# Optimization experiments

Hardware: AMD Instinct MI355X
Metric: run time of the kernel (lower is better)

## Reference

```python
import jax, jax.numpy as jnp
import numpy as np

B, L, E, H, W = 2, 8192, 1024, 16, 128
HD = E // H  # 64


def setup_inputs() -> dict:
    key = jax.random.key(0)
    ks = jax.random.split(key, 9)
    s = 1.0 / np.sqrt(E)
    inp = {"x": jax.random.normal(ks[0], (B, L, E), jnp.float32)}
    for i, n in enumerate(["Wq", "Wk", "Wv", "Wo"]):
        inp[n] = jax.random.uniform(ks[1 + i], (E, E), jnp.float32, -s, s)
    for i, n in enumerate(["bq", "bk", "bv", "bo"]):
        inp[n] = jax.random.uniform(ks[5 + i], (E,), jnp.float32, -s, s)
    return inp


def _skew_prob(p, w):
    # (..., w, 2w+1) -> (..., w, 3w) with row i right-shifted by i:
    # out[..., i, i+j] = p[..., i, j]  (zeros elsewhere)
    lead = p.shape[:-2]
    M, Lc = p.shape[-2], p.shape[-1]
    p = jnp.pad(p, [(0, 0)] * len(lead) + [(0, 0), (0, M + 1)])
    p = p.reshape(*lead, M * (Lc + M + 1))[..., :-M].reshape(*lead, M, M + Lc)
    return p[..., :-1]


def _sliding_attend(q, k, v, w):
    # q,k,v: (b,h,l,d); banded attention, window w on each side (2w+1 diagonals)
    b, h, l, d = q.shape
    c = l // w
    qc = q.reshape(b, h, c, w, d)
    # per-chunk key/value windows of 3w tokens (w halo each side, zero padded)
    idx = jnp.arange(c)[:, None] * w + jnp.arange(3 * w)[None, :]  # (c, 3w)
    kw = jnp.pad(k, ((0, 0), (0, 0), (w, w), (0, 0)))[:, :, idx]  # (b,h,c,3w,d)
    s = jnp.einsum('bhcqd,bhckd->bhcqk', qc, kw)  # (b,h,c,w,3w)
    # extract band: band[i, j] = s[i, i+j], j in [0, 2w] (offset d = j - w)
    gidx = (jnp.arange(w)[:, None] + jnp.arange(2 * w + 1)[None, :])[None, None, None]
    band = jnp.take_along_axis(s, gidx, axis=-1).reshape(b, h, l, 2 * w + 1)
    # mask out-of-range positions (matches the module's edge -inf loop)
    pos = jnp.arange(l)[:, None] + (jnp.arange(2 * w + 1) - w)[None, :]
    band = jnp.where((pos >= 0) & (pos < l), band, -jnp.inf)
    prob = jax.nn.softmax(band / np.sqrt(d), axis=-1)  # scale by sqrt(head_dim)
    vw = jnp.pad(v, ((0, 0), (0, 0), (w, w), (0, 0)))[:, :, idx]  # (b,h,c,3w,d)
    p3 = _skew_prob(prob.reshape(b, h, c, w, 2 * w + 1), w)  # (b,h,c,w,3w)
    ctx = jnp.einsum('bhcqk,bhckd->bhcqd', p3, vw)
    return ctx.reshape(b, h, l, d)


def reference(x, Wq, Wk, Wv, Wo, bq, bk, bv, bo):
    q = (x @ Wq.T + bq).reshape(B, L, H, HD).transpose(0, 2, 1, 3)
    k = (x @ Wk.T + bk).reshape(B, L, H, HD).transpose(0, 2, 1, 3)
    v = (x @ Wv.T + bv).reshape(B, L, H, HD).transpose(0, 2, 1, 3)
    ctx = _sliding_attend(q, k, v, W)
    ctx = ctx.transpose(0, 2, 1, 3).reshape(B, L, E)
    return ctx @ Wo.T + bo
```

## Files before the change

kernel.cpp:

```cpp
#include <hip/hip_runtime.h>
#include <math.h>

#define B_SZ  2
#define L_SEQ 8192
#define EMB   1024
#define NH    16
#define HDIM  64
#define WIN   128
#define MROWS (B_SZ*L_SEQ)

typedef __attribute__((ext_vector_type(8))) _Float16 f16x8;
typedef __attribute__((ext_vector_type(4))) _Float16 f16x4;
typedef __attribute__((ext_vector_type(4))) float f32x4;

__device__ __forceinline__ void gload16(const void* g, void* l) {
    __builtin_amdgcn_global_load_lds(
        (const __attribute__((address_space(1))) unsigned int*)g,
        (__attribute__((address_space(3))) unsigned int*)l, 16, 0, 0);
}

__global__ __launch_bounds__(256)
void round_all(const float* __restrict__ x,
               const float* __restrict__ wq, const float* __restrict__ wk,
               const float* __restrict__ wv, const float* __restrict__ wo,
               _Float16* __restrict__ xf, _Float16* __restrict__ q16,
               _Float16* __restrict__ k16, _Float16* __restrict__ v16,
               _Float16* __restrict__ o16)
{
    const size_t NX = (size_t)MROWS * EMB, NW = (size_t)EMB * EMB;
    size_t gid = ((size_t)blockIdx.x * 256 + threadIdx.x) * 4;
    const float* src; _Float16* dst; size_t off;
    if (gid < NX)               { src = x;  dst = xf;  off = gid; }
    else if (gid < NX + NW)     { src = wq; dst = q16; off = gid - NX; }
    else if (gid < NX + 2*NW)   { src = wk; dst = k16; off = gid - NX - 2*NW + NW; }
    else if (gid < NX + 3*NW)   { src = wv; dst = v16; off = gid - NX - 2*NW; }
    else                        { src = wo; dst = o16; off = gid - NX - 3*NW; }
    float4 v = *(const float4*)(src + off);
    f16x4 o;
    o[0] = (_Float16)v.x; o[1] = (_Float16)v.y;
    o[2] = (_Float16)v.z; o[3] = (_Float16)v.w;
    *(f16x4*)(dst + off) = o;
}


#define STAGE_HT(ptr_, tb_, op_, h_, kt_)                                      \
    {                                                                          \
        char* d_ = smem + (op_) * 65536 + ((kt_) & 1) * 32768 + (h_) * 16384 + ldst; \
        const _Float16* s_ = (ptr_) + ((size_t)((tb_) + (h_) * 128 + srow6)) * 1024 + (kt_) * 64 + gch; \
        gload16(s_, d_);                                                       \
        gload16(s_ + 64 * 1024, d_ + 8192);                                    \
    }

#define DSREAD_A(qr_)                                                          \
    _Pragma("unroll")                                                          \
    for (int i_ = 0; i_ < 4; ++i_) {                                           \
        const int ro_ = (qr_) * 8192 + (i_ * 16 + frow) * 128;                 \
        af[i_][0] = *(const f16x8*)(Ab + ro_ + sb0);                           \
        af[i_][1] = *(const f16x8*)(Ab + ro_ + sb1);                           \
    }

#define DSREAD_B_TO(dst_, qc_)                                                 \
    _Pragma("unroll")                                                          \
    for (int j_ = 0; j_ < 2; ++j_) {                                           \
        const int ro_ = (brow + (qc_) * 32 + j_ * 16 + frow) * 128;            \
        dst_[j_][0] = *(const f16x8*)(Bb + ro_ + sb0);                         \
        dst_[j_][1] = *(const f16x8*)(Bb + ro_ + sb1);                         \
    }

#define MFMA16(qr_, qc_, barr_)                                                \
    __builtin_amdgcn_s_setprio(1);                                             \
    _Pragma("unroll")                                                          \
    for (int ks_ = 0; ks_ < 2; ++ks_)                                          \
        _Pragma("unroll")                                                      \
        for (int i_ = 0; i_ < 4; ++i_)                                         \
            _Pragma("unroll")                                                  \
            for (int j_ = 0; j_ < 2; ++j_)                                     \
                acc[(qr_) * 4 + i_][(qc_) * 2 + j_] =                          \
                    __builtin_amdgcn_mfma_f32_16x16x32_f16(                    \
                        af[i_][ks_], barr_[j_][ks_],                           \
                        acc[(qr_) * 4 + i_][(qc_) * 2 + j_], 0, 0, 0);         \
    __builtin_amdgcn_s_setprio(0);

#define BARM()                                                                 \
    asm volatile("" ::: "memory");                                             \
    __builtin_amdgcn_s_barrier();                                              \
    asm volatile("" ::: "memory");

#define GEMM8_CORE(Aptr, Bptr)                                                 \
    const int t = threadIdx.x;                                                 \
    const int wave = t >> 6, lane = t & 63;                                    \
    const int wr = wave >> 2, wc = wave & 3;                                   \
    const int frow = lane & 15, quad = lane >> 4;                              \
    const int srow6 = t >> 3;                                                  \
    const int gch = ((t & 7) ^ (srow6 & 7)) * 8;                               \
    const int ldst = t * 16;                                                   \
    const int sb0 = (quad ^ (frow & 7)) * 16, sb1 = sb0 ^ 64;                  \
    const int brow = (wc & 1) * 64;                                            \
    f32x4 acc[8][4] = {};                                                      \
    f16x8 af[4][2], bfA[2][2], bfB[2][2];                                      \
    STAGE_HT(Aptr, bm, 0, 0, 0) STAGE_HT(Aptr, bm, 0, 1, 0)                    \
    STAGE_HT(Bptr, bn, 1, 0, 0) STAGE_HT(Bptr, bn, 1, 1, 0)                    \
    for (int kt = 0; kt < 16; ++kt) {                                          \
        const char* Ab = smem + (kt & 1) * 32768 + wr * 16384;                 \
        const char* Bb = smem + 65536 + (kt & 1) * 32768 + (wc >> 1) * 16384;  \
        if (kt < 15) {                                                         \
            STAGE_HT(Aptr, bm, 0, 0, kt + 1)                                   \
            asm volatile("s_waitcnt vmcnt(2)" ::: "memory");                   \
        } else {                                                               \
            asm volatile("s_waitcnt vmcnt(0)" ::: "memory");                   \
        }                                                                      \
        BARM()                                                                 \
        DSREAD_A(0) DSREAD_B_TO(bfA, 0)          \
        MFMA16(0, 0, bfA)                                                      \
        DSREAD_B_TO(bfB, 1)                    \
        if (kt < 15) STAGE_HT(Aptr, bm, 0, 1, kt + 1)                          \
        BARM()                                                                 \
        MFMA16(0, 1, bfB)                                                      \
        DSREAD_A(1)                                                            \
        if (kt < 15) STAGE_HT(Bptr, bn, 1, 0, kt + 1)                          \
        BARM()                                                                 \
        MFMA16(1, 1, bfB)                                                      \
        if (kt < 15) STAGE_HT(Bptr, bn, 1, 1, kt + 1)                          \
        BARM()                                                                 \
        MFMA16(1, 0, bfA)                     \
        BARM()                                                                 \
    }

__global__ __launch_bounds__(512, 2)
void gemm_qkv(const _Float16* __restrict__ X,
              const _Float16* __restrict__ Wq, const _Float16* __restrict__ Wk,
              const _Float16* __restrict__ Wv,
              const float* __restrict__ bq, const float* __restrict__ bk,
              const float* __restrict__ bv,
              _Float16* __restrict__ qf, _Float16* __restrict__ kf,
              _Float16* __restrict__ vtf)
{
    __shared__ __attribute__((aligned(16))) char smem[131072];

    const int id = blockIdx.x;
    const int row = (id / 96) * 8 + (id & 7);
    const int colq = (id >> 3) % 12;
    const int wsel = colq >> 2;
    const int bm = row * 256, bn = (colq & 3) * 256;
    const _Float16* Bw = wsel == 0 ? Wq : wsel == 1 ? Wk : Wv;
    const float* bias = wsel == 0 ? bq : wsel == 1 ? bk : bv;
    const float scale = wsel == 0 ? 0.18033688011112042f : 1.0f;

    GEMM8_CORE(X, Bw)

    char* Cw = smem + wave * 8192;
    const int bb = bm >> 13;
    const int l0 = (bm & (L_SEQ - 1)) + wr * 128;
    const int h = (bn >> 6) + wc;
    if (wsel < 2) {
        _Float16* dst = wsel == 0 ? qf : kf;
        const size_t hb = ((size_t)(bb * NH + h)) * L_SEQ * HDIM;
        #pragma unroll
        for (int ih = 0; ih < 2; ++ih) {
            asm volatile("" ::: "memory");
            #pragma unroll
            for (int i = 0; i < 4; ++i)
                #pragma unroll
                for (int j = 0; j < 4; ++j) {
                    const int lc = j * 16 + frow;
                    const float bvv = bias[bn + wc * 64 + lc];
                    #pragma unroll
                    for (int r = 0; r < 4; ++r) {
                        const int lr = i * 16 + quad * 4 + r;
                        const int bo = lr * 128 + ((lc * 2) ^ ((lr & 7) << 4));
                        *(_Float16*)(Cw + bo) = (_Float16)((acc[ih * 4 + i][j][r] + bvv) * scale);
                    }
                }
            asm volatile("" ::: "memory");
            #pragma unroll
            for (int p = 0; p < 8; ++p) {
                const int idx = p * 64 + lane;
                const int lr = idx >> 3, seg = idx & 7;
                const int bo = lr * 128 + ((seg * 16) ^ ((lr & 7) << 4));
                uint4 v = *(const uint4*)(Cw + bo);
                *(uint4*)&dst[hb + (size_t)(l0 + ih * 64 + lr) * HDIM + seg * 8] = v;
            }
        }
    } else {
        const size_t hb = ((size_t)(bb * NH + h)) * HDIM * L_SEQ;
        #pragma unroll
        for (int ih = 0; ih < 2; ++ih) {
            asm volatile("" ::: "memory");
            #pragma unroll
            for (int i = 0; i < 4; ++i)
                #pragma unroll
                for (int j = 0; j < 4; ++j) {
                    const int lc = j * 16 + frow;
                    const float bvv = bias[bn + wc * 64 + lc];
                    #pragma unroll
                    for (int r = 0; r < 4; ++r) {
                        const int lr = i * 16 + quad * 4 + r;
                        const int bo = lc * 128 + ((lr * 2) ^ ((lc & 7) << 4));
                        *(_Float16*)(Cw + bo) = (_Float16)(acc[ih * 4 + i][j][r] + bvv);
                    }
                }
            asm volatile("" ::: "memory");
            #pragma unroll
            for (int p = 0; p < 8; ++p) {
                const int idx = p * 64 + lane;
                const int dc = idx >> 3, sl = idx & 7;
                const int bo = dc * 128 + ((sl * 16) ^ ((dc & 7) << 4));
                uint4 v = *(const uint4*)(Cw + bo);
                *(uint4*)&vtf[hb + (size_t)dc * L_SEQ + (l0 + ih * 64 + sl * 8)] = v;
            }
        }
    }
}

__global__ __launch_bounds__(512, 2)
void gemm_out(const _Float16* __restrict__ A, const _Float16* __restrict__ Bwm,
              const float* __restrict__ bias, float* __restrict__ C)
{
    constexpr int N = EMB;
    __shared__ __attribute__((aligned(16))) char smem[131072];

    const int id = blockIdx.x;
    const int row = (id / 32) * 8 + (id & 7);
    const int bm = row * 256, bn = ((id >> 3) & 3) * 256;

    GEMM8_CORE(A, Bwm)

    #pragma unroll
    for (int i = 0; i < 8; ++i) {
        int m0 = bm + wr * 128 + i * 16 + quad * 4;
        #pragma unroll
        for (int j = 0; j < 4; ++j) {
            int n = bn + wc * 64 + j * 16 + frow;
            float bvv = bias[n];
            #pragma unroll
            for (int r = 0; r < 4; ++r)
                C[(size_t)(m0 + r) * N + n] = acc[i][j][r] + bvv;
        }
    }
}

__global__ __launch_bounds__(1024)
void attn_mfma(const _Float16* __restrict__ qf, const _Float16* __restrict__ kf,
               const _Float16* __restrict__ vtf, _Float16* __restrict__ cf)
{
    __shared__ _Float16 Kt[8][4096];
    __shared__ _Float16 Vt[8][4096];

    const int t = threadIdx.x;
    const int wave = t >> 6, lane = t & 63;
    const int col = lane & 15, quad = lane >> 4;
    const int bh = blockIdx.y;
    const int xi = blockIdx.x;
    const int xq = (xi & 7) * 4 + (xi >> 3);
    const int q0 = xq * 256;
    const int oo = wave * 16;

    const int tk = t & 511;
    const int srow = tk >> 3, sc = tk & 7;
    const int gq = sc ^ (srow & 7);
    #pragma unroll
    for (int kt = 0; kt < 8; kt++) {
        const int p0s = q0 - WIN + kt * 64;
        if (p0s < 0 || p0s > L_SEQ - 64) continue;
        if (t < 512) {
            size_t kgi = ((size_t)bh * L_SEQ + p0s + srow) * HDIM + gq * 8;
            gload16(kf + kgi, (char*)&Kt[kt][0] + tk * 16);
        } else {
            size_t vgi = ((size_t)bh * HDIM + srow) * L_SEQ + p0s + gq * 8;
            gload16(vtf + vgi, (char*)&Vt[kt][0] + tk * 16);
        }
    }

    f16x8 qfr[2];
    {
        size_t qidx = ((size_t)bh * L_SEQ + q0 + oo + col) * HDIM + quad * 8;
        qfr[0] = *(const f16x8*)(qf + qidx);
        qfr[1] = *(const f16x8*)(qf + qidx + 32);
    }

    asm volatile("s_waitcnt vmcnt(0)" ::: "memory");
    __builtin_amdgcn_s_barrier();
    asm volatile("" ::: "memory");

    f32x4 o[4] = {};
    f32x4 o5 = {};
    const f16x4 vones = {(_Float16)1.0f, (_Float16)1.0f,
                         (_Float16)1.0f, (_Float16)1.0f};

    #pragma unroll
    for (int kt = 0; kt < 8; kt++) {
        const int p0 = q0 - WIN + kt * 64;
        if (p0 < 0 || p0 > L_SEQ - 64) continue;
        const int relp = kt * 64 - WIN - oo;
        if (relp < -191 || relp > 143) continue;

        const char* Kb = (const char*)&Kt[kt][0];
        const char* Vb = (const char*)&Vt[kt][0];

        f32x4 sT[4] = {};
        __builtin_amdgcn_s_setprio(1);
        #pragma unroll
        for (int ks = 0; ks < 2; ks++)
            #pragma unroll
            for (int n = 0; n < 4; n++) {
                int off = (n * 16 + col) * 128 + (((ks * 4 + quad) ^ (col & 7)) * 16);
                f16x8 kfr = *(const f16x8*)(Kb + off);
                sT[n] = __builtin_amdgcn_mfma_f32_16x16x32_f16(kfr, qfr[ks], sT[n], 0, 0, 0);
            }
        __builtin_amdgcn_s_setprio(0);
        if (relp < -113 || relp > 65) {
            const int qrow = q0 + oo + col;
            #pragma unroll
            for (int n = 0; n < 4; n++)
                #pragma unroll
                for (int r = 0; r < 4; r++) {
                    int dlt = (p0 + n * 16 + quad * 4 + r) - qrow;
                    if (dlt < -WIN || dlt > WIN) sT[n][r] = -3e38f;
                }
        }
        f16x4 pT[4];
        #pragma unroll
        for (int n = 0; n < 4; n++)
            #pragma unroll
            for (int r = 0; r < 4; r++)
                pT[n][r] = (_Float16)__builtin_amdgcn_exp2f(sT[n][r]);
        __builtin_amdgcn_s_setprio(1);
        #pragma unroll
        for (int n = 0; n < 4; n++)
            o5 = __builtin_amdgcn_mfma_f32_16x16x16f16(vones, pT[n], o5, 0, 0, 0);
        #pragma unroll
        for (int m = 0; m < 4; m++) {
            #pragma unroll
            for (int n = 0; n < 4; n++) {
                int off = (m * 16 + col) * 128 +
                          (((2 * n + (quad >> 1)) ^ (col & 7)) * 16) + (quad & 1) * 8;
                f16x4 vfr = *(const f16x4*)(Vb + off);
                o[m] = __builtin_amdgcn_mfma_f32_16x16x16f16(vfr, pT[n], o[m], 0, 0, 0);
            }
        }
        __builtin_amdgcn_s_setprio(0);
    }

    const float inv = 1.0f / o5[0];

    const int b = bh >> 4, h = bh & 15;
    const size_t base = ((size_t)b * L_SEQ + q0 + oo + col) * EMB + h * HDIM;
    #pragma unroll
    for (int m = 0; m < 4; m++) {
        f16x4 ov;
        #pragma unroll
        for (int r = 0; r < 4; r++) ov[r] = (_Float16)(o[m][r] * inv);
        *(f16x4*)&cf[base + m * 16 + quad * 4] = ov;
    }
}

extern "C" void kernel_launch(void* const* d_in, const int* in_sizes, int n_in,
                              void* d_out, int out_size, void* d_ws, size_t ws_size,
                              hipStream_t stream) {
    const float* x  = (const float*)d_in[0];
    const float* Wq = (const float*)d_in[1];
    const float* Wk = (const float*)d_in[2];
    const float* Wv = (const float*)d_in[3];
    const float* Wo = (const float*)d_in[4];
    const float* bq = (const float*)d_in[5];
    const float* bk = (const float*)d_in[6];
    const float* bv = (const float*)d_in[7];
    const float* bo = (const float*)d_in[8];
    float* out = (float*)d_out;

    const size_t per = (size_t)B_SZ * NH * L_SEQ * HDIM;
    _Float16* w16 = (_Float16*)d_ws;
    _Float16* xf   = w16;
    _Float16* qf   = w16 + per;
    _Float16* kf   = w16 + 2 * per;
    _Float16* vtf  = w16 + 3 * per;
    _Float16* cf   = w16 + 4 * per;
    _Float16* wq16 = w16 + 5 * per;
    _Float16* wk16 = wq16 + 1048576;
    _Float16* wv16 = wq16 + 2 * 1048576;
    _Float16* wo16 = wq16 + 3 * 1048576;

    const int nround = (MROWS * EMB + 4 * EMB * EMB) / 1024;
    round_all<<<nround, dim3(256), 0, stream>>>(x, Wq, Wk, Wv, Wo, xf, wq16, wk16, wv16, wo16);

    gemm_qkv<<<768, dim3(512), 0, stream>>>(xf, wq16, wk16, wv16, bq, bk, bv, qf, kf, vtf);

    attn_mfma<<<dim3(L_SEQ / 256, B_SZ * NH), dim3(1024), 0, stream>>>(qf, kf, vtf, cf);

    gemm_out<<<256, dim3(512), 0, stream>>>(cf, wo16, bo, out);
}
```

Baseline: 322.5 us.

## Double-buffer K/V tiles in attention and halve block size to 128 queries

The attention kernel now processes 128 queries per block with 512 threads instead of 256 queries with 1024 threads. Rather than loading all eight K/V tiles up front into 128KB of LDS, it stages pairs of 64-key tiles into a two-slot double buffer and overlaps loading the next pair with computing the current one. This cuts LDS use per block, which may let more blocks share a CU and hides global-load latency. The cost is extra barriers per stage and some redundant halo K/V loads, since neighbouring blocks now overlap more.

```diff
diff --git a/kernel.cpp b/kernel.cpp
--- a/kernel.cpp
+++ b/kernel.cpp
@@ -239,37 +239,39 @@
     }
 }
 
-__global__ __launch_bounds__(1024)
+__global__ __launch_bounds__(512)
 void attn_mfma(const _Float16* __restrict__ qf, const _Float16* __restrict__ kf,
                const _Float16* __restrict__ vtf, _Float16* __restrict__ cf)
 {
-    __shared__ _Float16 Kt[8][4096];
-    __shared__ _Float16 Vt[8][4096];
+    __shared__ _Float16 Kt[2][2][4096];
+    __shared__ _Float16 Vt[2][2][4096];
 
     const int t = threadIdx.x;
     const int wave = t >> 6, lane = t & 63;
     const int col = lane & 15, quad = lane >> 4;
     const int bh = blockIdx.y;
     const int xi = blockIdx.x;
-    const int xq = (xi & 7) * 4 + (xi >> 3);
-    const int q0 = xq * 256;
+    const int xq = (xi & 7) * 8 + (xi >> 3);
+    const int q0 = xq * 128;
     const int oo = wave * 16;
 
-    const int tk = t & 511;
-    const int srow = tk >> 3, sc = tk & 7;
+    const int srow = t >> 3, sc = t & 7;
     const int gq = sc ^ (srow & 7);
-    #pragma unroll
-    for (int kt = 0; kt < 8; kt++) {
-        const int p0s = q0 - WIN + kt * 64;
-        if (p0s < 0 || p0s > L_SEQ - 64) continue;
-        if (t < 512) {
-            size_t kgi = ((size_t)bh * L_SEQ + p0s + srow) * HDIM + gq * 8;
-            gload16(kf + kgi, (char*)&Kt[kt][0] + tk * 16);
-        } else {
-            size_t vgi = ((size_t)bh * HDIM + srow) * L_SEQ + p0s + gq * 8;
-            gload16(vtf + vgi, (char*)&Vt[kt][0] + tk * 16);
-        }
-    }
+
+#define STAGE_PAIR(pt_, buf_)                                                  \
+    {                                                                          \
+        _Pragma("unroll")                                                      \
+        for (int j_ = 0; j_ < 2; ++j_) {                                       \
+            int p0s = q0 - WIN + ((pt_) + j_) * 64;                            \
+            p0s = p0s < 0 ? 0 : (p0s > L_SEQ - 64 ? L_SEQ - 64 : p0s);         \
+            size_t kgi = ((size_t)bh * L_SEQ + p0s + srow) * HDIM + gq * 8;    \
+            size_t vgi = ((size_t)bh * HDIM + srow) * L_SEQ + p0s + gq * 8;    \
+            gload16(kf + kgi, (char*)&Kt[buf_][j_][0] + t * 16);               \
+            gload16(vtf + vgi, (char*)&Vt[buf_][j_][0] + t * 16);              \
+        }                                                                      \
+    }
+
+    STAGE_PAIR(0, 0)
 
     f16x8 qfr[2];
     {
@@ -278,67 +280,79 @@
         qfr[1] = *(const f16x8*)(qf + qidx + 32);
     }
 
-    asm volatile("s_waitcnt vmcnt(0)" ::: "memory");
-    __builtin_amdgcn_s_barrier();
-    asm volatile("" ::: "memory");
-
     f32x4 o[4] = {};
     f32x4 o5 = {};
     const f16x4 vones = {(_Float16)1.0f, (_Float16)1.0f,
                          (_Float16)1.0f, (_Float16)1.0f};
 
     #pragma unroll
-    for (int kt = 0; kt < 8; kt++) {
-        const int p0 = q0 - WIN + kt * 64;
-        if (p0 < 0 || p0 > L_SEQ - 64) continue;
-        const int relp = kt * 64 - WIN - oo;
-        if (relp < -191 || relp > 143) continue;
-
-        const char* Kb = (const char*)&Kt[kt][0];
-        const char* Vb = (const char*)&Vt[kt][0];
-
-        f32x4 sT[4] = {};
-        __builtin_amdgcn_s_setprio(1);
+    for (int s = 0; s < 3; ++s) {
+        if (s < 2) {
+            STAGE_PAIR(2 * (s + 1), (s + 1) & 1)
+            asm volatile("s_waitcnt vmcnt(4)" ::: "memory");
+        } else {
+            asm volatile("s_waitcnt vmcnt(0)" ::: "memory");
+        }
+        __builtin_amdgcn_s_barrier();
+        asm volatile("" ::: "memory");
+
         #pragma unroll
-        for (int ks = 0; ks < 2; ks++)
-            #pragma unroll
-            for (int n = 0; n < 4; n++) {
-                int off = (n * 16 + col) * 128 + (((ks * 4 + quad) ^ (col & 7)) * 16);
-                f16x8 kfr = *(const f16x8*)(Kb + off);
-                sT[n] = __builtin_amdgcn_mfma_f32_16x16x32_f16(kfr, qfr[ks], sT[n], 0, 0, 0);
+        for (int j = 0; j < 2; ++j) {
+            const int kt = 2 * s + j;
+            const int p0 = q0 - WIN + kt * 64;
+            if (p0 < 0 || p0 > L_SEQ - 64) continue;
+            const int relp = kt * 64 - WIN - oo;
+            if (relp < -191 || relp > 143) continue;
+
+            const char* Kb = (const char*)&Kt[s & 1][j][0];
+            const char* Vb = (const char*)&Vt[s & 1][j][0];
+
+            f32x4 sT[4] = {};
+            __builtin_amdgcn_s_setprio(1);
+            #pragma unroll
+            for (int ks = 0; ks < 2; ks++)
+                #pragma unroll
+                for (int n = 0; n < 4; n++) {
+                    int off = (n * 16 + col) * 128 + (((ks * 4 + quad) ^ (col & 7)) * 16);
+                    f16x8 kfr = *(const f16x8*)(Kb + off);
+                    sT[n] = __builtin_amdgcn_mfma_f32_16x16x32_f16(kfr, qfr[ks], sT[n], 0, 0, 0);
+                }
+            __builtin_amdgcn_s_setprio(0);
+            if (relp < -113 || relp > 65) {
+                const int qrow = q0 + oo + col;
+                #pragma unroll
+                for (int n = 0; n < 4; n++)
+                    #pragma unroll
+                    for (int r = 0; r < 4; r++) {
+                        int dlt = (p0 + n * 16 + quad * 4 + r) - qrow;
+                        if (dlt < -WIN || dlt > WIN) sT[n][r] = -3e38f;
+                    }
             }
-        __builtin_amdgcn_s_setprio(0);
-        if (relp < -113 || relp > 65) {
-            const int qrow = q0 + oo + col;
+            f16x4 pT[4];
             #pragma unroll
             for (int n = 0; n < 4; n++)
                 #pragma unroll
-                for (int r = 0; r < 4; r++) {
-                    int dlt = (p0 + n * 16 + quad * 4 + r) - qrow;
-                    if (dlt < -WIN || dlt > WIN) sT[n][r] = -3e38f;
+                for (int r = 0; r < 4; r++)
+                    pT[n][r] = (_Float16)__builtin_amdgcn_exp2f(sT[n][r]);
+            __builtin_amdgcn_s_setprio(1);
+            #pragma unroll
+            for (int n = 0; n < 4; n++)
+                o5 = __builtin_amdgcn_mfma_f32_16x16x16f16(vones, pT[n], o5, 0, 0, 0);
+            #pragma unroll
+            for (int m = 0; m < 4; m++) {
+                #pragma unroll
+                for (int n = 0; n < 4; n++) {
+                    int off = (m * 16 + col) * 128 +
+                              (((2 * n + (quad >> 1)) ^ (col & 7)) * 16) + (quad & 1) * 8;
+                    f16x4 vfr = *(const f16x4*)(Vb + off);
+                    o[m] = __builtin_amdgcn_mfma_f32_16x16x16f16(vfr, pT[n], o[m], 0, 0, 0);
                 }
+            }
+            __builtin_amdgcn_s_setprio(0);
         }
-        f16x4 pT[4];
-        #pragma unroll
-        for (int n = 0; n < 4; n++)
-            #pragma unroll
-            for (int r = 0; r < 4; r++)
-                pT[n][r] = (_Float16)__builtin_amdgcn_exp2f(sT[n][r]);
-        __builtin_amdgcn_s_setprio(1);
-        #pragma unroll
-        for (int n = 0; n < 4; n++)
-            o5 = __builtin_amdgcn_mfma_f32_16x16x16f16(vones, pT[n], o5, 0, 0, 0);
-        #pragma unroll
-        for (int m = 0; m < 4; m++) {
-            #pragma unroll
-            for (int n = 0; n < 4; n++) {
-                int off = (m * 16 + col) * 128 +
-                          (((2 * n + (quad >> 1)) ^ (col & 7)) * 16) + (quad & 1) * 8;
-                f16x4 vfr = *(const f16x4*)(Vb + off);
-                o[m] = __builtin_amdgcn_mfma_f32_16x16x16f16(vfr, pT[n], o[m], 0, 0, 0);
-            }
-        }
-        __builtin_amdgcn_s_setprio(0);
+        asm volatile("" ::: "memory");
+        __builtin_amdgcn_s_barrier();
+        asm volatile("" ::: "memory");
     }
 
     const float inv = 1.0f / o5[0];
@@ -385,7 +399,7 @@
 
     gemm_qkv<<<768, dim3(512), 0, stream>>>(xf, wq16, wk16, wv16, bq, bk, bv, qf, kf, vtf);
 
-    attn_mfma<<<dim3(L_SEQ / 256, B_SZ * NH), dim3(1024), 0, stream>>>(qf, kf, vtf, cf);
+    attn_mfma<<<dim3(L_SEQ / 128, B_SZ * NH), dim3(512), 0, stream>>>(qf, kf, vtf, cf);
 
     gemm_out<<<256, dim3(512), 0, stream>>>(cf, wo16, bo, out);
 }
```

After: 329.4 us. 1.02x slower.
